# Performance work log

Hardware: AMD Instinct MI355X
Metric: run time of the kernel (lower is better)

Reference implementation:

```python
import jax, jax.numpy as jnp
import numpy as np
from jax import lax

HEADS = 8
DIM_HEAD = 64


def _conv1d(x, w, b):
    # x: (B, C_in, L), w: (C_out, C_in, K), valid padding, stride 1
    y = lax.conv_general_dilated(x, w, window_strides=(1,), padding='VALID',
                                 dimension_numbers=('NCH', 'OIH', 'NCH'))
    return y + b[None, :, None]


def setup_inputs() -> dict:
    key = jax.random.key(0)
    ks = jax.random.split(key, 8)
    B, N, D = 4, 2048, 64
    inner = HEADS * DIM_HEAD  # 512
    x = jax.random.normal(ks[0], (B, N, D), jnp.float32)
    W_qk = jax.random.normal(ks[1], (2 * inner, D), jnp.float32) * (1.0 / np.sqrt(D))
    w_conv1 = jax.random.normal(ks[2], (2, 1, 25), jnp.float32) * 0.2
    b_conv1 = jax.random.normal(ks[3], (2,), jnp.float32) * 0.01
    w_conv2 = jax.random.normal(ks[4], (4, 2, 10), jnp.float32) * 0.2
    b_conv2 = jax.random.normal(ks[5], (4,), jnp.float32) * 0.01
    W_out = jax.random.normal(ks[6], (D, 992), jnp.float32) * (1.0 / np.sqrt(992))
    b_out = jax.random.normal(ks[7], (D,), jnp.float32) * 0.01
    return {'x': x, 'W_qk': W_qk, 'w_conv1': w_conv1, 'b_conv1': b_conv1,
            'w_conv2': w_conv2, 'b_conv2': b_conv2, 'W_out': W_out, 'b_out': b_out}


def reference(x, W_qk, w_conv1, b_conv1, w_conv2, b_conv2, W_out, b_out):
    B, N, D = x.shape
    H, Dh = HEADS, DIM_HEAD
    scale = Dh ** -0.5
    # Q, K projection: Linear(dim, 2*inner, bias=False)
    qk = x @ W_qk.T                       # (B, N, 2*H*Dh)
    q, k = jnp.split(qk, 2, axis=-1)
    q = q.reshape(B, N, H, Dh).transpose(0, 2, 1, 3)  # (B, H, N, Dh)
    k = k.reshape(B, N, H, Dh).transpose(0, 2, 1, 3)
    # Convalue: two valid 1D convs along the feature axis (64 -> 40 -> 31, C 1->2->4).
    # Original loops over heads with the SAME weights, so compute once and broadcast.
    xc = x.reshape(B * N, 1, D)
    h1 = _conv1d(xc, w_conv1, b_conv1)    # (B*N, 2, 40)
    h2 = _conv1d(h1, w_conv2, b_conv2)    # (B*N, 4, 31)
    v = h2.reshape(B, N, -1)              # (B, N, 124) == (c d) per head
    # Attention (dropout = 0.0)
    dots = jnp.einsum('bhid,bhjd->bhij', q, k) * scale   # (B, H, N, N)
    attn = jax.nn.softmax(dots, axis=-1)
    out = jnp.einsum('bhij,bjd->bhid', attn, v)          # (B, H, N, 124)
    out = out.transpose(0, 2, 1, 3).reshape(B, N, H * v.shape[-1])  # (B, N, 992)
    out = out @ W_out.T + b_out           # (B, N, dim)
    return out, attn
```

## Files before the change

kernel.cpp:

```cpp
#include <hip/hip_runtime.h>

typedef _Float16 half8 __attribute__((ext_vector_type(8)));
typedef float f32x4 __attribute__((ext_vector_type(4)));

#define MFMA16(a, b, c) __builtin_amdgcn_mfma_f32_16x16x32_f16(a, b, c, 0, 0, 0)

__global__ void init_out_kernel(const float* __restrict__ bout, float* __restrict__ out) {
    int i = blockIdx.x * 256 + threadIdx.x;
    out[i] = bout[i & 63];
}

__global__ __launch_bounds__(256) void qk_proj_kernel(
    const float* __restrict__ x, const float* __restrict__ Wqk,
    _Float16* __restrict__ qhi, _Float16* __restrict__ qlo,
    _Float16* __restrict__ khi, _Float16* __restrict__ klo)
{
    __shared__ float4 xs[128][16];
    int t = threadIdx.x;
    int oc = blockIdx.x & 3;
    int rowblk = blockIdx.x >> 2;
    int row0 = rowblk * 128;
    int o = oc * 256 + t;

    float4 wr[16];
    const float4* wp = (const float4*)(Wqk + o * 64);
#pragma unroll
    for (int j = 0; j < 16; ++j) wr[j] = wp[j];

    const float4* xsrc = (const float4*)(x + (size_t)row0 * 64);
#pragma unroll
    for (int i = 0; i < 8; ++i) {
        int idx = t + i * 256;
        xs[idx >> 4][idx & 15] = xsrc[idx];
    }
    __syncthreads();

    bool isq = o < 512;
    int oo = isq ? o : o - 512;
    int h = oo >> 6, d = oo & 63;
    float scl = isq ? 0.125f : 1.0f;
    _Float16* hp = isq ? qhi : khi;
    _Float16* lp = isq ? qlo : klo;

    for (int r = 0; r < 128; ++r) {
        float acc = 0.f;
#pragma unroll
        for (int j = 0; j < 16; ++j) {
            float4 xv = xs[r][j];
            float4 wv = wr[j];
            acc += xv.x * wv.x + xv.y * wv.y + xv.z * wv.z + xv.w * wv.w;
        }
        float val = acc * scl;
        _Float16 hi = (_Float16)val;
        _Float16 lo = (_Float16)(val - (float)hi);
        int row = row0 + r;
        int b = row >> 11, n = row & 2047;
        size_t idx = ((size_t)((b * 8 + h) * 2048 + n) << 6) + d;
        hp[idx] = hi;
        lp[idx] = lo;
    }
}

__global__ __launch_bounds__(256) void conv_v_kernel(
    const float* __restrict__ x,
    const float* __restrict__ w1, const float* __restrict__ b1,
    const float* __restrict__ w2, const float* __restrict__ b2,
    _Float16* __restrict__ vt)
{
    __shared__ float xs[16][64];
    __shared__ float h1[16][80];
    __shared__ float cw1[50], cb1[2], cw2[80], cb2[4];
    int t = threadIdx.x;
    int row0 = blockIdx.x * 16;

    ((float4*)&xs[0][0])[t] = ((const float4*)(x + (size_t)row0 * 64))[t];
    if (t < 50) cw1[t] = w1[t];
    else if (t < 52) cb1[t - 50] = b1[t - 50];
    else if (t < 132) cw2[t - 52] = w2[t - 52];
    else if (t < 136) cb2[t - 132] = b2[t - 132];
    __syncthreads();

    for (int it = t; it < 1280; it += 256) {
        int r = it / 80, rem = it % 80;
        int ch = rem / 40, tt = rem % 40;
        float acc = cb1[ch];
#pragma unroll
        for (int k = 0; k < 25; ++k) acc += xs[r][tt + k] * cw1[ch * 25 + k];
        h1[r][ch * 40 + tt] = acc;
    }
    __syncthreads();

    int b = row0 >> 11, n0 = row0 & 2047;
    for (int it = t; it < 2048; it += 256) {
        int r = it >> 7, c = it & 127;
        float val = 0.f;
        if (c < 124) {
            int co = c / 31, tt = c % 31;
            float acc = cb2[co];
#pragma unroll
            for (int ci = 0; ci < 2; ++ci)
#pragma unroll
                for (int k = 0; k < 10; ++k)
                    acc += h1[r][ci * 40 + tt + k] * cw2[(co * 2 + ci) * 10 + k];
            val = acc;
        }
        vt[((size_t)(b * 128 + c) << 11) + n0 + r] = (_Float16)val;
    }
}

__global__ __launch_bounds__(256, 3) void attn_kernel(
    const _Float16* __restrict__ qhi_g, const _Float16* __restrict__ qlo_g,
    const _Float16* __restrict__ khi_g, const _Float16* __restrict__ klo_g,
    const _Float16* __restrict__ vt_g, const float* __restrict__ Wout,
    float* __restrict__ outp, float* __restrict__ attn)
{
    __shared__ __align__(16) char smem[46080];
    _Float16* KHI = (_Float16*)smem;
    _Float16* KLO = (_Float16*)(smem + 9216);
    _Float16* VT  = (_Float16*)(smem + 18432);

    int t = threadIdx.x;
    int w = t >> 6, lane = t & 63, quad = lane >> 4, m = lane & 15;
    _Float16* PB = (_Float16*)(smem + 36864) + w * 1152;

    int ib = blockIdx.x;
    int bh = (ib & 7) * 4 + ((ib >> 3) & 3);
    int rowblk = ib >> 5;
    int b = bh >> 3, h = bh & 7;
    int row0 = rowblk * 64;

    const size_t qoff = ((size_t)(bh * 2048 + row0 + w * 16 + m)) << 6;
    half8 qh[2], ql[2];
    qh[0] = *(const half8*)(qhi_g + qoff + quad * 8);
    qh[1] = *(const half8*)(qhi_g + qoff + quad * 8 + 32);
    ql[0] = *(const half8*)(qlo_g + qoff + quad * 8);
    ql[1] = *(const half8*)(qlo_g + qoff + quad * 8 + 32);

    const size_t kbase = ((size_t)(bh * 2048)) << 6;

    float ls0 = 0.f, ls1 = 0.f, ls2 = 0.f, ls3 = 0.f;
    for (int tile = 0; tile < 32; ++tile) {
        __syncthreads();
        const _Float16* ks = khi_g + kbase + (size_t)tile * (64 * 64);
        const _Float16* lsrc = klo_g + kbase + (size_t)tile * (64 * 64);
#pragma unroll
        for (int rep = 0; rep < 2; ++rep) {
            int c = t + rep * 256;
            int key = c >> 3, seg = c & 7;
            *(half8*)(KHI + key * 72 + seg * 8) = *(const half8*)(ks + key * 64 + seg * 8);
            *(half8*)(KLO + key * 72 + seg * 8) = *(const half8*)(lsrc + key * 64 + seg * 8);
        }
        __syncthreads();
#pragma unroll
        for (int chunk = 0; chunk < 4; ++chunk) {
            f32x4 acc = {0.f, 0.f, 0.f, 0.f};
#pragma unroll
            for (int dh = 0; dh < 2; ++dh) {
                half8 bhv = *(const half8*)(KHI + (chunk * 16 + m) * 72 + dh * 32 + quad * 8);
                half8 blv = *(const half8*)(KLO + (chunk * 16 + m) * 72 + dh * 32 + quad * 8);
                acc = MFMA16(qh[dh], bhv, acc);
                acc = MFMA16(ql[dh], bhv, acc);
                acc = MFMA16(qh[dh], blv, acc);
            }
            ls0 += __expf(acc[0]); ls1 += __expf(acc[1]);
            ls2 += __expf(acc[2]); ls3 += __expf(acc[3]);
        }
    }
#pragma unroll
    for (int mask = 1; mask <= 8; mask <<= 1) {
        ls0 += __shfl_xor(ls0, mask);
        ls1 += __shfl_xor(ls1, mask);
        ls2 += __shfl_xor(ls2, mask);
        ls3 += __shfl_xor(ls3, mask);
    }
    float ri0 = 1.f / ls0, ri1 = 1.f / ls1, ri2 = 1.f / ls2, ri3 = 1.f / ls3;

    f32x4 oacc[8];
#pragma unroll
    for (int cc = 0; cc < 8; ++cc) oacc[cc] = (f32x4){0.f, 0.f, 0.f, 0.f};
    float* attn_b = attn + (((size_t)bh) << 22);
    const _Float16* vs_base = vt_g + (((size_t)b * 128) << 11);

    for (int tile = 0; tile < 32; ++tile) {
        __syncthreads();
        const _Float16* ks = khi_g + kbase + (size_t)tile * (64 * 64);
        const _Float16* lsrc = klo_g + kbase + (size_t)tile * (64 * 64);
#pragma unroll
        for (int rep = 0; rep < 2; ++rep) {
            int c = t + rep * 256;
            int key = c >> 3, seg = c & 7;
            *(half8*)(KHI + key * 72 + seg * 8) = *(const half8*)(ks + key * 64 + seg * 8);
            *(half8*)(KLO + key * 72 + seg * 8) = *(const half8*)(lsrc + key * 64 + seg * 8);
        }
#pragma unroll
        for (int rep = 0; rep < 4; ++rep) {
            int c = t + rep * 256;
            int ch = c >> 3, seg = c & 7;
            *(half8*)(VT + ch * 72 + seg * 8) =
                *(const half8*)(vs_base + (size_t)ch * 2048 + tile * 64 + seg * 8);
        }
        __syncthreads();

        int n0t = tile * 64;
#pragma unroll
        for (int chunk = 0; chunk < 4; ++chunk) {
            f32x4 acc = {0.f, 0.f, 0.f, 0.f};
#pragma unroll
            for (int dh = 0; dh < 2; ++dh) {
                half8 bhv = *(const half8*)(KHI + (chunk * 16 + m) * 72 + dh * 32 + quad * 8);
                half8 blv = *(const half8*)(KLO + (chunk * 16 + m) * 72 + dh * 32 + quad * 8);
                acc = MFMA16(qh[dh], bhv, acc);
                acc = MFMA16(ql[dh], bhv, acc);
                acc = MFMA16(qh[dh], blv, acc);
            }
            int col = n0t + chunk * 16 + m;
            int rg = row0 + w * 16 + quad * 4;
            float p0 = __expf(acc[0]) * ri0;
            float p1 = __expf(acc[1]) * ri1;
            float p2 = __expf(acc[2]) * ri2;
            float p3 = __expf(acc[3]) * ri3;
            __builtin_nontemporal_store(p0, attn_b + (size_t)(rg + 0) * 2048 + col);
            __builtin_nontemporal_store(p1, attn_b + (size_t)(rg + 1) * 2048 + col);
            __builtin_nontemporal_store(p2, attn_b + (size_t)(rg + 2) * 2048 + col);
            __builtin_nontemporal_store(p3, attn_b + (size_t)(rg + 3) * 2048 + col);
            PB[(quad * 4 + 0) * 72 + chunk * 16 + m] = (_Float16)p0;
            PB[(quad * 4 + 1) * 72 + chunk * 16 + m] = (_Float16)p1;
            PB[(quad * 4 + 2) * 72 + chunk * 16 + m] = (_Float16)p2;
            PB[(quad * 4 + 3) * 72 + chunk * 16 + m] = (_Float16)p3;
        }
#pragma unroll
        for (int kk = 0; kk < 2; ++kk) {
            half8 a = *(const half8*)(PB + m * 72 + kk * 32 + quad * 8);
#pragma unroll
            for (int cc = 0; cc < 8; ++cc) {
                half8 bv = *(const half8*)(VT + (cc * 16 + m) * 72 + kk * 32 + quad * 8);
                oacc[cc] = MFMA16(a, bv, oacc[cc]);
            }
        }
    }

    __syncthreads();
    float* o_lds = (float*)smem;
#pragma unroll
    for (int cc = 0; cc < 8; ++cc)
#pragma unroll
        for (int r = 0; r < 4; ++r)
            o_lds[(w * 16 + quad * 4 + r) * 132 + cc * 16 + m] = oacc[cc][r];
    __syncthreads();

    int d = t & 63, rg2 = t >> 6;
    const float* wrow = Wout + d * 992 + h * 124;
    for (int rr = 0; rr < 16; ++rr) {
        int row = rg2 + rr * 4;
        const float* orow = o_lds + row * 132;
        float acc = 0.f;
#pragma unroll
        for (int c4 = 0; c4 < 31; ++c4) {
            float4 wv = ((const float4*)wrow)[c4];
            float4 ov = ((const float4*)orow)[c4];
            acc += ov.x * wv.x + ov.y * wv.y + ov.z * wv.z + ov.w * wv.w;
        }
        atomicAdd(outp + ((size_t)(b * 2048 + row0 + row) << 6) + d, acc);
    }
}

extern "C" void kernel_launch(void* const* d_in, const int* in_sizes, int n_in,
                              void* d_out, int out_size, void* d_ws, size_t ws_size,
                              hipStream_t stream) {
    const float* x    = (const float*)d_in[0];
    const float* Wqk  = (const float*)d_in[1];
    const float* w1   = (const float*)d_in[2];
    const float* b1   = (const float*)d_in[3];
    const float* w2   = (const float*)d_in[4];
    const float* b2   = (const float*)d_in[5];
    const float* Wout = (const float*)d_in[6];
    const float* bout = (const float*)d_in[7];

    float* out  = (float*)d_out;
    float* attn = out + 524288;

    _Float16* ws  = (_Float16*)d_ws;
    _Float16* qhi = ws;
    _Float16* qlo = ws + 4194304;
    _Float16* khi = ws + 8388608;
    _Float16* klo = ws + 12582912;
    _Float16* vt  = ws + 16777216;

    init_out_kernel<<<2048, 256, 0, stream>>>(bout, out);
    qk_proj_kernel<<<256, 256, 0, stream>>>(x, Wqk, qhi, qlo, khi, klo);
    conv_v_kernel<<<512, 256, 0, stream>>>(x, w1, b1, w2, b2, vt);
    attn_kernel<<<1024, 256, 0, stream>>>(qhi, qlo, khi, klo, vt, Wout, out, attn);
}
```

Before: 829.4 us.

## Load K and V fragments directly from global memory instead of staging in LDS

The attention kernel stops cooperatively staging K hi/lo and V tiles in shared memory. Each lane now reads its MFMA operand fragments straight from global memory, which removes the per-tile block barriers and most of the LDS footprint, and launch bounds are raised to allow 4 blocks per CU. The QK projection kernel is also split into smaller 64-row blocks to double its grid. The trade-off is that every wave re-reads K and V from global memory or cache rather than sharing one LDS copy, which raises L2 traffic and exposes load latency that the block no longer hides through cooperative staging.

```diff
diff --git a/kernel.cpp b/kernel.cpp
--- a/kernel.cpp
+++ b/kernel.cpp
@@ -15,11 +15,11 @@
     _Float16* __restrict__ qhi, _Float16* __restrict__ qlo,
     _Float16* __restrict__ khi, _Float16* __restrict__ klo)
 {
-    __shared__ float4 xs[128][16];
+    __shared__ float4 xs[64][16];
     int t = threadIdx.x;
     int oc = blockIdx.x & 3;
     int rowblk = blockIdx.x >> 2;
-    int row0 = rowblk * 128;
+    int row0 = rowblk * 64;
     int o = oc * 256 + t;
 
     float4 wr[16];
@@ -29,7 +29,7 @@
 
     const float4* xsrc = (const float4*)(x + (size_t)row0 * 64);
 #pragma unroll
-    for (int i = 0; i < 8; ++i) {
+    for (int i = 0; i < 4; ++i) {
         int idx = t + i * 256;
         xs[idx >> 4][idx & 15] = xsrc[idx];
     }
@@ -42,7 +42,7 @@
     _Float16* hp = isq ? qhi : khi;
     _Float16* lp = isq ? qlo : klo;
 
-    for (int r = 0; r < 128; ++r) {
+    for (int r = 0; r < 64; ++r) {
         float acc = 0.f;
 #pragma unroll
         for (int j = 0; j < 16; ++j) {
@@ -108,20 +108,17 @@
     }
 }
 
-__global__ __launch_bounds__(256, 3) void attn_kernel(
+__global__ __launch_bounds__(256, 4) void attn_kernel(
     const _Float16* __restrict__ qhi_g, const _Float16* __restrict__ qlo_g,
     const _Float16* __restrict__ khi_g, const _Float16* __restrict__ klo_g,
     const _Float16* __restrict__ vt_g, const float* __restrict__ Wout,
     float* __restrict__ outp, float* __restrict__ attn)
 {
-    __shared__ __align__(16) char smem[46080];
-    _Float16* KHI = (_Float16*)smem;
-    _Float16* KLO = (_Float16*)(smem + 9216);
-    _Float16* VT  = (_Float16*)(smem + 18432);
+    __shared__ __align__(16) char smem[33792];
 
     int t = threadIdx.x;
     int w = t >> 6, lane = t & 63, quad = lane >> 4, m = lane & 15;
-    _Float16* PB = (_Float16*)(smem + 36864) + w * 1152;
+    _Float16* PB = (_Float16*)smem + w * 1152;
 
     int ib = blockIdx.x;
     int bh = (ib & 7) * 4 + ((ib >> 3) & 3);
@@ -136,28 +133,21 @@
     ql[0] = *(const half8*)(qlo_g + qoff + quad * 8);
     ql[1] = *(const half8*)(qlo_g + qoff + quad * 8 + 32);
 
-    const size_t kbase = ((size_t)(bh * 2048)) << 6;
+    const size_t kbase = (((size_t)(bh * 2048)) << 6) + (size_t)m * 64 + quad * 8;
+    const _Float16* kh_base = khi_g + kbase;
+    const _Float16* kl_base = klo_g + kbase;
 
     float ls0 = 0.f, ls1 = 0.f, ls2 = 0.f, ls3 = 0.f;
     for (int tile = 0; tile < 32; ++tile) {
-        __syncthreads();
-        const _Float16* ks = khi_g + kbase + (size_t)tile * (64 * 64);
-        const _Float16* lsrc = klo_g + kbase + (size_t)tile * (64 * 64);
-#pragma unroll
-        for (int rep = 0; rep < 2; ++rep) {
-            int c = t + rep * 256;
-            int key = c >> 3, seg = c & 7;
-            *(half8*)(KHI + key * 72 + seg * 8) = *(const half8*)(ks + key * 64 + seg * 8);
-            *(half8*)(KLO + key * 72 + seg * 8) = *(const half8*)(lsrc + key * 64 + seg * 8);
-        }
-        __syncthreads();
+        const _Float16* kh = kh_base + tile * 4096;
+        const _Float16* kl = kl_base + tile * 4096;
 #pragma unroll
         for (int chunk = 0; chunk < 4; ++chunk) {
             f32x4 acc = {0.f, 0.f, 0.f, 0.f};
 #pragma unroll
             for (int dh = 0; dh < 2; ++dh) {
-                half8 bhv = *(const half8*)(KHI + (chunk * 16 + m) * 72 + dh * 32 + quad * 8);
-                half8 blv = *(const half8*)(KLO + (chunk * 16 + m) * 72 + dh * 32 + quad * 8);
+                half8 bhv = *(const half8*)(kh + chunk * 1024 + dh * 32);
+                half8 blv = *(const half8*)(kl + chunk * 1024 + dh * 32);
                 acc = MFMA16(qh[dh], bhv, acc);
                 acc = MFMA16(ql[dh], bhv, acc);
                 acc = MFMA16(qh[dh], blv, acc);
@@ -179,36 +169,19 @@
 #pragma unroll
     for (int cc = 0; cc < 8; ++cc) oacc[cc] = (f32x4){0.f, 0.f, 0.f, 0.f};
     float* attn_b = attn + (((size_t)bh) << 22);
-    const _Float16* vs_base = vt_g + (((size_t)b * 128) << 11);
+    const _Float16* v_base = vt_g + (((size_t)(b * 128 + m)) << 11) + quad * 8;
 
     for (int tile = 0; tile < 32; ++tile) {
-        __syncthreads();
-        const _Float16* ks = khi_g + kbase + (size_t)tile * (64 * 64);
-        const _Float16* lsrc = klo_g + kbase + (size_t)tile * (64 * 64);
-#pragma unroll
-        for (int rep = 0; rep < 2; ++rep) {
-            int c = t + rep * 256;
-            int key = c >> 3, seg = c & 7;
-            *(half8*)(KHI + key * 72 + seg * 8) = *(const half8*)(ks + key * 64 + seg * 8);
-            *(half8*)(KLO + key * 72 + seg * 8) = *(const half8*)(lsrc + key * 64 + seg * 8);
-        }
-#pragma unroll
-        for (int rep = 0; rep < 4; ++rep) {
-            int c = t + rep * 256;
-            int ch = c >> 3, seg = c & 7;
-            *(half8*)(VT + ch * 72 + seg * 8) =
-                *(const half8*)(vs_base + (size_t)ch * 2048 + tile * 64 + seg * 8);
-        }
-        __syncthreads();
-
+        const _Float16* kh = kh_base + tile * 4096;
+        const _Float16* kl = kl_base + tile * 4096;
         int n0t = tile * 64;
 #pragma unroll
         for (int chunk = 0; chunk < 4; ++chunk) {
             f32x4 acc = {0.f, 0.f, 0.f, 0.f};
 #pragma unroll
             for (int dh = 0; dh < 2; ++dh) {
-                half8 bhv = *(const half8*)(KHI + (chunk * 16 + m) * 72 + dh * 32 + quad * 8);
-                half8 blv = *(const half8*)(KLO + (chunk * 16 + m) * 72 + dh * 32 + quad * 8);
+                half8 bhv = *(const half8*)(kh + chunk * 1024 + dh * 32);
+                half8 blv = *(const half8*)(kl + chunk * 1024 + dh * 32);
                 acc = MFMA16(qh[dh], bhv, acc);
                 acc = MFMA16(ql[dh], bhv, acc);
                 acc = MFMA16(qh[dh], blv, acc);
@@ -233,7 +206,7 @@
             half8 a = *(const half8*)(PB + m * 72 + kk * 32 + quad * 8);
 #pragma unroll
             for (int cc = 0; cc < 8; ++cc) {
-                half8 bv = *(const half8*)(VT + (cc * 16 + m) * 72 + kk * 32 + quad * 8);
+                half8 bv = *(const half8*)(v_base + ((size_t)cc << 15) + n0t + kk * 32);
                 oacc[cc] = MFMA16(a, bv, oacc[cc]);
             }
         }
@@ -287,7 +260,7 @@
     _Float16* vt  = ws + 16777216;
 
     init_out_kernel<<<2048, 256, 0, stream>>>(bout, out);
-    qk_proj_kernel<<<256, 256, 0, stream>>>(x, Wqk, qhi, qlo, khi, klo);
+    qk_proj_kernel<<<512, 256, 0, stream>>>(x, Wqk, qhi, qlo, khi, klo);
     conv_v_kernel<<<512, 256, 0, stream>>>(x, w1, b1, w2, b2, vt);
     attn_kernel<<<1024, 256, 0, stream>>>(qhi, qlo, khi, klo, vt, Wout, out, attn);
 }
```

After: 1.248 ms. +50.5%, slower.

## Process two query row tiles per attention block to reuse K/V tiles

Applied to the files above, without the earlier changes.

Each attention block now handles 128 query rows (two 64-row groups) instead of 64. Each K and V tile loaded into LDS is reused across twice as many MFMAs, which halves the K/V global-to-LDS traffic and the two-pass recomputation overhead per row. This doubles accumulator and register state, lowers occupancy to 2 blocks and halves the grid to 512 blocks. The QK projection also switches to 64-row blocks with twice the grid, to spread its work across more blocks.

```diff
diff --git a/kernel.cpp b/kernel.cpp
--- a/kernel.cpp
+++ b/kernel.cpp
@@ -15,11 +15,11 @@
     _Float16* __restrict__ qhi, _Float16* __restrict__ qlo,
     _Float16* __restrict__ khi, _Float16* __restrict__ klo)
 {
-    __shared__ float4 xs[128][16];
+    __shared__ float4 xs[64][16];
     int t = threadIdx.x;
     int oc = blockIdx.x & 3;
     int rowblk = blockIdx.x >> 2;
-    int row0 = rowblk * 128;
+    int row0 = rowblk * 64;
     int o = oc * 256 + t;
 
     float4 wr[16];
@@ -29,7 +29,7 @@
 
     const float4* xsrc = (const float4*)(x + (size_t)row0 * 64);
 #pragma unroll
-    for (int i = 0; i < 8; ++i) {
+    for (int i = 0; i < 4; ++i) {
         int idx = t + i * 256;
         xs[idx >> 4][idx & 15] = xsrc[idx];
     }
@@ -42,7 +42,7 @@
     _Float16* hp = isq ? qhi : khi;
     _Float16* lp = isq ? qlo : klo;
 
-    for (int r = 0; r < 128; ++r) {
+    for (int r = 0; r < 64; ++r) {
         float acc = 0.f;
 #pragma unroll
         for (int j = 0; j < 16; ++j) {
@@ -108,37 +108,45 @@
     }
 }
 
-__global__ __launch_bounds__(256, 3) void attn_kernel(
+__global__ __launch_bounds__(256, 2) void attn_kernel(
     const _Float16* __restrict__ qhi_g, const _Float16* __restrict__ qlo_g,
     const _Float16* __restrict__ khi_g, const _Float16* __restrict__ klo_g,
     const _Float16* __restrict__ vt_g, const float* __restrict__ Wout,
     float* __restrict__ outp, float* __restrict__ attn)
 {
-    __shared__ __align__(16) char smem[46080];
+    __shared__ __align__(16) char smem[55296];
     _Float16* KHI = (_Float16*)smem;
     _Float16* KLO = (_Float16*)(smem + 9216);
     _Float16* VT  = (_Float16*)(smem + 18432);
 
     int t = threadIdx.x;
     int w = t >> 6, lane = t & 63, quad = lane >> 4, m = lane & 15;
-    _Float16* PB = (_Float16*)(smem + 36864) + w * 1152;
+    _Float16* PB0 = (_Float16*)(smem + 36864) + w * 2304;
+    _Float16* PB1 = PB0 + 1152;
 
     int ib = blockIdx.x;
     int bh = (ib & 7) * 4 + ((ib >> 3) & 3);
     int rowblk = ib >> 5;
     int b = bh >> 3, h = bh & 7;
-    int row0 = rowblk * 64;
-
-    const size_t qoff = ((size_t)(bh * 2048 + row0 + w * 16 + m)) << 6;
-    half8 qh[2], ql[2];
-    qh[0] = *(const half8*)(qhi_g + qoff + quad * 8);
-    qh[1] = *(const half8*)(qhi_g + qoff + quad * 8 + 32);
-    ql[0] = *(const half8*)(qlo_g + qoff + quad * 8);
-    ql[1] = *(const half8*)(qlo_g + qoff + quad * 8 + 32);
+    int row0 = rowblk * 128;
+
+    const size_t qoff0 = ((size_t)(bh * 2048 + row0 + w * 16 + m)) << 6;
+    const size_t qoff1 = qoff0 + (size_t)(64 << 6);
+    half8 qh0[2], ql0[2], qh1[2], ql1[2];
+    qh0[0] = *(const half8*)(qhi_g + qoff0 + quad * 8);
+    qh0[1] = *(const half8*)(qhi_g + qoff0 + quad * 8 + 32);
+    ql0[0] = *(const half8*)(qlo_g + qoff0 + quad * 8);
+    ql0[1] = *(const half8*)(qlo_g + qoff0 + quad * 8 + 32);
+    qh1[0] = *(const half8*)(qhi_g + qoff1 + quad * 8);
+    qh1[1] = *(const half8*)(qhi_g + qoff1 + quad * 8 + 32);
+    ql1[0] = *(const half8*)(qlo_g + qoff1 + quad * 8);
+    ql1[1] = *(const half8*)(qlo_g + qoff1 + quad * 8 + 32);
 
     const size_t kbase = ((size_t)(bh * 2048)) << 6;
 
-    float ls0 = 0.f, ls1 = 0.f, ls2 = 0.f, ls3 = 0.f;
+    float ls[8];
+#pragma unroll
+    for (int i = 0; i < 8; ++i) ls[i] = 0.f;
     for (int tile = 0; tile < 32; ++tile) {
         __syncthreads();
         const _Float16* ks = khi_g + kbase + (size_t)tile * (64 * 64);
@@ -153,31 +161,40 @@
         __syncthreads();
 #pragma unroll
         for (int chunk = 0; chunk < 4; ++chunk) {
-            f32x4 acc = {0.f, 0.f, 0.f, 0.f};
+            f32x4 a0 = {0.f, 0.f, 0.f, 0.f};
+            f32x4 a1 = {0.f, 0.f, 0.f, 0.f};
 #pragma unroll
             for (int dh = 0; dh < 2; ++dh) {
                 half8 bhv = *(const half8*)(KHI + (chunk * 16 + m) * 72 + dh * 32 + quad * 8);
                 half8 blv = *(const half8*)(KLO + (chunk * 16 + m) * 72 + dh * 32 + quad * 8);
-                acc = MFMA16(qh[dh], bhv, acc);
-                acc = MFMA16(ql[dh], bhv, acc);
-                acc = MFMA16(qh[dh], blv, acc);
+                a0 = MFMA16(qh0[dh], bhv, a0);
+                a0 = MFMA16(ql0[dh], bhv, a0);
+                a0 = MFMA16(qh0[dh], blv, a0);
+                a1 = MFMA16(qh1[dh], bhv, a1);
+                a1 = MFMA16(ql1[dh], bhv, a1);
+                a1 = MFMA16(qh1[dh], blv, a1);
             }
-            ls0 += __expf(acc[0]); ls1 += __expf(acc[1]);
-            ls2 += __expf(acc[2]); ls3 += __expf(acc[3]);
+            ls[0] += __expf(a0[0]); ls[1] += __expf(a0[1]);
+            ls[2] += __expf(a0[2]); ls[3] += __expf(a0[3]);
+            ls[4] += __expf(a1[0]); ls[5] += __expf(a1[1]);
+            ls[6] += __expf(a1[2]); ls[7] += __expf(a1[3]);
         }
     }
 #pragma unroll
     for (int mask = 1; mask <= 8; mask <<= 1) {
-        ls0 += __shfl_xor(ls0, mask);
-        ls1 += __shfl_xor(ls1, mask);
-        ls2 += __shfl_xor(ls2, mask);
-        ls3 += __shfl_xor(ls3, mask);
-    }
-    float ri0 = 1.f / ls0, ri1 = 1.f / ls1, ri2 = 1.f / ls2, ri3 = 1.f / ls3;
-
-    f32x4 oacc[8];
-#pragma unroll
-    for (int cc = 0; cc < 8; ++cc) oacc[cc] = (f32x4){0.f, 0.f, 0.f, 0.f};
+#pragma unroll
+        for (int i = 0; i < 8; ++i) ls[i] += __shfl_xor(ls[i], mask);
+    }
+    float ri[8];
+#pragma unroll
+    for (int i = 0; i < 8; ++i) ri[i] = 1.f / ls[i];
+
+    f32x4 oacc0[8], oacc1[8];
+#pragma unroll
+    for (int cc = 0; cc < 8; ++cc) {
+        oacc0[cc] = (f32x4){0.f, 0.f, 0.f, 0.f};
+        oacc1[cc] = (f32x4){0.f, 0.f, 0.f, 0.f};
+    }
     float* attn_b = attn + (((size_t)bh) << 22);
     const _Float16* vs_base = vt_g + (((size_t)b * 128) << 11);
 
@@ -204,63 +221,86 @@
         int n0t = tile * 64;
 #pragma unroll
         for (int chunk = 0; chunk < 4; ++chunk) {
-            f32x4 acc = {0.f, 0.f, 0.f, 0.f};
+            f32x4 a0 = {0.f, 0.f, 0.f, 0.f};
+            f32x4 a1 = {0.f, 0.f, 0.f, 0.f};
 #pragma unroll
             for (int dh = 0; dh < 2; ++dh) {
                 half8 bhv = *(const half8*)(KHI + (chunk * 16 + m) * 72 + dh * 32 + quad * 8);
                 half8 blv = *(const half8*)(KLO + (chunk * 16 + m) * 72 + dh * 32 + quad * 8);
-                acc = MFMA16(qh[dh], bhv, acc);
-                acc = MFMA16(ql[dh], bhv, acc);
-                acc = MFMA16(qh[dh], blv, acc);
+                a0 = MFMA16(qh0[dh], bhv, a0);
+                a0 = MFMA16(ql0[dh], bhv, a0);
+                a0 = MFMA16(qh0[dh], blv, a0);
+                a1 = MFMA16(qh1[dh], bhv, a1);
+                a1 = MFMA16(ql1[dh], bhv, a1);
+                a1 = MFMA16(qh1[dh], blv, a1);
             }
             int col = n0t + chunk * 16 + m;
-            int rg = row0 + w * 16 + quad * 4;
-            float p0 = __expf(acc[0]) * ri0;
-            float p1 = __expf(acc[1]) * ri1;
-            float p2 = __expf(acc[2]) * ri2;
-            float p3 = __expf(acc[3]) * ri3;
-            __builtin_nontemporal_store(p0, attn_b + (size_t)(rg + 0) * 2048 + col);
-            __builtin_nontemporal_store(p1, attn_b + (size_t)(rg + 1) * 2048 + col);
-            __builtin_nontemporal_store(p2, attn_b + (size_t)(rg + 2) * 2048 + col);
-            __builtin_nontemporal_store(p3, attn_b + (size_t)(rg + 3) * 2048 + col);
-            PB[(quad * 4 + 0) * 72 + chunk * 16 + m] = (_Float16)p0;
-            PB[(quad * 4 + 1) * 72 + chunk * 16 + m] = (_Float16)p1;
-            PB[(quad * 4 + 2) * 72 + chunk * 16 + m] = (_Float16)p2;
-            PB[(quad * 4 + 3) * 72 + chunk * 16 + m] = (_Float16)p3;
+            int rg0 = row0 + w * 16 + quad * 4;
+            int rg1 = rg0 + 64;
+            float p00 = __expf(a0[0]) * ri[0];
+            float p01 = __expf(a0[1]) * ri[1];
+            float p02 = __expf(a0[2]) * ri[2];
+            float p03 = __expf(a0[3]) * ri[3];
+            float p10 = __expf(a1[0]) * ri[4];
+            float p11 = __expf(a1[1]) * ri[5];
+            float p12 = __expf(a1[2]) * ri[6];
+            float p13 = __expf(a1[3]) * ri[7];
+            __builtin_nontemporal_store(p00, attn_b + (size_t)(rg0 + 0) * 2048 + col);
+            __builtin_nontemporal_store(p01, attn_b + (size_t)(rg0 + 1) * 2048 + col);
+            __builtin_nontemporal_store(p02, attn_b + (size_t)(rg0 + 2) * 2048 + col);
+            __builtin_nontemporal_store(p03, attn_b + (size_t)(rg0 + 3) * 2048 + col);
+            __builtin_nontemporal_store(p10, attn_b + (size_t)(rg1 + 0) * 2048 + col);
+            __builtin_nontemporal_store(p11, attn_b + (size_t)(rg1 + 1) * 2048 + col);
+            __builtin_nontemporal_store(p12, attn_b + (size_t)(rg1 + 2) * 2048 + col);
+            __builtin_nontemporal_store(p13, attn_b + (size_t)(rg1 + 3) * 2048 + col);
+            PB0[(quad * 4 + 0) * 72 + chunk * 16 + m] = (_Float16)p00;
+            PB0[(quad * 4 + 1) * 72 + chunk * 16 + m] = (_Float16)p01;
+            PB0[(quad * 4 + 2) * 72 + chunk * 16 + m] = (_Float16)p02;
+            PB0[(quad * 4 + 3) * 72 + chunk * 16 + m] = (_Float16)p03;
+            PB1[(quad * 4 + 0) * 72 + chunk * 16 + m] = (_Float16)p10;
+            PB1[(quad * 4 + 1) * 72 + chunk * 16 + m] = (_Float16)p11;
+            PB1[(quad * 4 + 2) * 72 + chunk * 16 + m] = (_Float16)p12;
+            PB1[(quad * 4 + 3) * 72 + chunk * 16 + m] = (_Float16)p13;
         }
 #pragma unroll
         for (int kk = 0; kk < 2; ++kk) {
-            half8 a = *(const half8*)(PB + m * 72 + kk * 32 + quad * 8);
+            half8 a0 = *(const half8*)(PB0 + m * 72 + kk * 32 + quad * 8);
+            half8 a1 = *(const half8*)(PB1 + m * 72 + kk * 32 + quad * 8);
 #pragma unroll
             for (int cc = 0; cc < 8; ++cc) {
                 half8 bv = *(const half8*)(VT + (cc * 16 + m) * 72 + kk * 32 + quad * 8);
-                oacc[cc] = MFMA16(a, bv, oacc[cc]);
+                oacc0[cc] = MFMA16(a0, bv, oacc0[cc]);
+                oacc1[cc] = MFMA16(a1, bv, oacc1[cc]);
             }
         }
     }
 
-    __syncthreads();
     float* o_lds = (float*)smem;
-#pragma unroll
-    for (int cc = 0; cc < 8; ++cc)
-#pragma unroll
-        for (int r = 0; r < 4; ++r)
-            o_lds[(w * 16 + quad * 4 + r) * 132 + cc * 16 + m] = oacc[cc][r];
-    __syncthreads();
-
     int d = t & 63, rg2 = t >> 6;
     const float* wrow = Wout + d * 992 + h * 124;
-    for (int rr = 0; rr < 16; ++rr) {
-        int row = rg2 + rr * 4;
-        const float* orow = o_lds + row * 132;
-        float acc = 0.f;
-#pragma unroll
-        for (int c4 = 0; c4 < 31; ++c4) {
-            float4 wv = ((const float4*)wrow)[c4];
-            float4 ov = ((const float4*)orow)[c4];
-            acc += ov.x * wv.x + ov.y * wv.y + ov.z * wv.z + ov.w * wv.w;
-        }
-        atomicAdd(outp + ((size_t)(b * 2048 + row0 + row) << 6) + d, acc);
+#pragma unroll
+    for (int g = 0; g < 2; ++g) {
+        __syncthreads();
+#pragma unroll
+        for (int cc = 0; cc < 8; ++cc)
+#pragma unroll
+            for (int r = 0; r < 4; ++r)
+                o_lds[(w * 16 + quad * 4 + r) * 132 + cc * 16 + m] =
+                    g ? oacc1[cc][r] : oacc0[cc][r];
+        __syncthreads();
+
+        for (int rr = 0; rr < 16; ++rr) {
+            int row = rg2 + rr * 4;
+            const float* orow = o_lds + row * 132;
+            float acc = 0.f;
+#pragma unroll
+            for (int c4 = 0; c4 < 31; ++c4) {
+                float4 wv = ((const float4*)wrow)[c4];
+                float4 ov = ((const float4*)orow)[c4];
+                acc += ov.x * wv.x + ov.y * wv.y + ov.z * wv.z + ov.w * wv.w;
+            }
+            atomicAdd(outp + ((size_t)(b * 2048 + row0 + g * 64 + row) << 6) + d, acc);
+        }
     }
 }
 
@@ -287,7 +327,7 @@
     _Float16* vt  = ws + 16777216;
 
     init_out_kernel<<<2048, 256, 0, stream>>>(bout, out);
-    qk_proj_kernel<<<256, 256, 0, stream>>>(x, Wqk, qhi, qlo, khi, klo);
+    qk_proj_kernel<<<512, 256, 0, stream>>>(x, Wqk, qhi, qlo, khi, klo);
     conv_v_kernel<<<512, 256, 0, stream>>>(x, w1, b1, w2, b2, vt);
-    attn_kernel<<<1024, 256, 0, stream>>>(qhi, qlo, khi, klo, vt, Wout, out, attn);
-}
+    attn_kernel<<<512, 256, 0, stream>>>(qhi, qlo, khi, klo, vt, Wout, out, attn);
+}
```

Result: faster. 782.9 us (-5.6%).
